# Kernel optimization log

Measured on AMD Instinct MI355X. Metric: run time of the kernel, lower is better.

## Reference

```python
import jax, jax.numpy as jnp
import numpy as np


def setup_inputs() -> dict:
    key = jax.random.key(0)
    k1, k2, k3, k4 = jax.random.split(key, 4)
    B, L, F, V = 512, 512, 64, 20000
    src_ids = jax.random.randint(k1, (B, L), 0, V, dtype=jnp.int32)
    dst_ids = jax.random.randint(k2, (B, L), 0, V, dtype=jnp.int32)
    # MLP params: Linear(1->F), ReLU, Linear(F->F)
    W1 = jax.random.normal(k3, (1, F), dtype=jnp.float32)  # fan_in = 1
    b1 = jnp.zeros((F,), dtype=jnp.float32)
    W2 = jax.random.normal(k4, (F, F), dtype=jnp.float32) * (1.0 / np.sqrt(F))
    b2 = jnp.zeros((F,), dtype=jnp.float32)
    return {"src_ids": src_ids, "dst_ids": dst_ids, "W1": W1, "b1": b1,
            "W2": W2, "b2": b2, "num_nodes": V}


def reference(src_ids, dst_ids, W1, b1, W2, b2, num_nodes):
    # Per-row histogram over node ids (vectorized replacement for
    # np.unique + dict gather in the torch code).
    row_hist = lambda r: jnp.bincount(r, length=num_nodes)
    hist_src = jax.vmap(row_hist)(src_ids)  # [B, V]
    hist_dst = jax.vmap(row_hist)(dst_ids)  # [B, V]

    gather = lambda h, ids: jnp.take_along_axis(h, ids, axis=1)  # [B, L]

    # appearances: [count in own seq, count in other seq], shape [B, L, 2]
    src_app = jnp.stack([gather(hist_src, src_ids), gather(hist_dst, src_ids)], axis=-1).astype(jnp.float32)
    dst_app = jnp.stack([gather(hist_src, dst_ids), gather(hist_dst, dst_ids)], axis=-1).astype(jnp.float32)
    # id 0 is padding -> zero both count channels
    src_app = jnp.where((src_ids == 0)[..., None], 0.0, src_app)
    dst_app = jnp.where((dst_ids == 0)[..., None], 0.0, dst_app)

    def encode(app):
        # app: [B, L, 2]; per-scalar MLP then sum over the 2 count channels
        h = jax.nn.relu(app[..., None] * W1[0] + b1)  # [B, L, 2, F]
        out = h @ W2 + b2                              # [B, L, 2, F]
        return out.sum(axis=2)                         # [B, L, F]

    return encode(src_app), encode(dst_app)
```

## Files before the change

kernel.cpp:

```cpp
#include <hip/hip_runtime.h>

constexpr int Bn = 512;
constexpr int Ln = 512;
constexpr int Fn = 64;
constexpr int Vn = 20000;
constexpr int HWORDS = (Vn + 2) / 3;

__global__ void build_table_kernel(const float* __restrict__ W1,
                                   const float* __restrict__ b1,
                                   const float* __restrict__ W2,
                                   const float* __restrict__ b2,
                                   float* __restrict__ table) {
    const int v = blockIdx.x;
    const int j = threadIdx.x;
    __shared__ float h[Fn];
    h[j] = fmaxf((float)v * W1[j] + b1[j], 0.0f);
    __syncthreads();
    float acc = b2[j];
#pragma unroll
    for (int i = 0; i < Fn; ++i)
        acc = fmaf(h[i], W2[i * Fn + j], acc);
    table[v * Fn + j] = acc;
}

__device__ __forceinline__ unsigned hist_get(const unsigned* __restrict__ h, int v) {
    const int w = v / 3;
    const int f = v - w * 3;
    return (h[w] >> (10 * f)) & 0x3FFu;
}

__global__ __launch_bounds__(256) void comco_kernel(
    const int* __restrict__ src_ids,
    const int* __restrict__ dst_ids,
    const float* __restrict__ table,
    float* __restrict__ out_src,
    float* __restrict__ out_dst) {
    __shared__ unsigned hs[HWORDS];
    __shared__ unsigned hd[HWORDS];

    const int b = blockIdx.x;
    const int tid = threadIdx.x;

    for (int i = tid; i < HWORDS; i += 256) { hs[i] = 0u; hd[i] = 0u; }
    __syncthreads();

    const int* __restrict__ srow = src_ids + b * Ln;
    const int* __restrict__ drow = dst_ids + b * Ln;

    for (int l = tid; l < Ln; l += 256) {
        const int s = srow[l];
        const int sw = s / 3;
        atomicAdd(&hs[sw], 1u << (10 * (s - sw * 3)));
        const int d = drow[l];
        const int dw = d / 3;
        atomicAdd(&hd[dw], 1u << (10 * (d - dw * 3)));
    }
    __syncthreads();

    const int g = tid >> 4;
    const int r = tid & 15;

    for (int l = g; l < Ln; l += 16) {
        const int sid = srow[l];
        const int did = drow[l];
        unsigned c_ss = 0, c_sd = 0, c_ds = 0, c_dd = 0;
        if (sid != 0) { c_ss = hist_get(hs, sid); c_sd = hist_get(hd, sid); }
        if (did != 0) { c_ds = hist_get(hs, did); c_dd = hist_get(hd, did); }

        const float4 t0 = *((const float4*)(table + c_ss * Fn) + r);
        const float4 t1 = *((const float4*)(table + c_sd * Fn) + r);
        const float4 u0 = *((const float4*)(table + c_ds * Fn) + r);
        const float4 u1 = *((const float4*)(table + c_dd * Fn) + r);

        float4 os, od;
        os.x = t0.x + t1.x; os.y = t0.y + t1.y; os.z = t0.z + t1.z; os.w = t0.w + t1.w;
        od.x = u0.x + u1.x; od.y = u0.y + u1.y; od.z = u0.z + u1.z; od.w = u0.w + u1.w;

        const size_t pos = (size_t)(b * Ln + l) * Fn;
        *((float4*)(out_src + pos) + r) = os;
        *((float4*)(out_dst + pos) + r) = od;
    }
}

extern "C" void kernel_launch(void* const* d_in, const int* in_sizes, int n_in,
                              void* d_out, int out_size, void* d_ws, size_t ws_size,
                              hipStream_t stream) {
    const int*   src_ids = (const int*)d_in[0];
    const int*   dst_ids = (const int*)d_in[1];
    const float* W1      = (const float*)d_in[2];
    const float* b1      = (const float*)d_in[3];
    const float* W2      = (const float*)d_in[4];
    const float* b2      = (const float*)d_in[5];

    float* table   = (float*)d_ws;
    float* out_src = (float*)d_out;
    float* out_dst = out_src + (size_t)Bn * Ln * Fn;

    build_table_kernel<<<Ln + 1, Fn, 0, stream>>>(W1, b1, W2, b2, table);
    comco_kernel<<<Bn, 256, 0, stream>>>(src_ids, dst_ids, table, out_src, out_dst);
}
```

Measured before the change: 150.1 us.

## Split histogram and output expansion into separate kernels via packed count buffer

The fused per-row kernel is split in two. A histogram kernel writes packed (own, other) counts per token to a workspace buffer, and a fully parallel expand kernel then gathers the two table rows and writes the output with one float4 per thread across the whole grid. This targets the low parallelism of the write phase, where 512 blocks each looped over 512 positions, and should let the large output store saturate bandwidth. The cost is an extra launch plus a small intermediate write and read of counts.

```diff
diff --git a/kernel.cpp b/kernel.cpp
--- a/kernel.cpp
+++ b/kernel.cpp
@@ -5,6 +5,7 @@
 constexpr int Fn = 64;
 constexpr int Vn = 20000;
 constexpr int HWORDS = (Vn + 2) / 3;
+constexpr int BL = Bn * Ln;
 
 __global__ void build_table_kernel(const float* __restrict__ W1,
                                    const float* __restrict__ b1,
@@ -29,12 +30,10 @@
     return (h[w] >> (10 * f)) & 0x3FFu;
 }
 
-__global__ __launch_bounds__(256) void comco_kernel(
+__global__ __launch_bounds__(256) void hist_kernel(
     const int* __restrict__ src_ids,
     const int* __restrict__ dst_ids,
-    const float* __restrict__ table,
-    float* __restrict__ out_src,
-    float* __restrict__ out_dst) {
+    unsigned* __restrict__ counts) {
     __shared__ unsigned hs[HWORDS];
     __shared__ unsigned hd[HWORDS];
 
@@ -47,39 +46,46 @@
     const int* __restrict__ srow = src_ids + b * Ln;
     const int* __restrict__ drow = dst_ids + b * Ln;
 
-    for (int l = tid; l < Ln; l += 256) {
-        const int s = srow[l];
-        const int sw = s / 3;
-        atomicAdd(&hs[sw], 1u << (10 * (s - sw * 3)));
-        const int d = drow[l];
-        const int dw = d / 3;
-        atomicAdd(&hd[dw], 1u << (10 * (d - dw * 3)));
+    const int s0 = srow[tid], s1 = srow[tid + 256];
+    const int d0 = drow[tid], d1 = drow[tid + 256];
+    {
+        int w;
+        w = s0 / 3; atomicAdd(&hs[w], 1u << (10 * (s0 - w * 3)));
+        w = s1 / 3; atomicAdd(&hs[w], 1u << (10 * (s1 - w * 3)));
+        w = d0 / 3; atomicAdd(&hd[w], 1u << (10 * (d0 - w * 3)));
+        w = d1 / 3; atomicAdd(&hd[w], 1u << (10 * (d1 - w * 3)));
     }
     __syncthreads();
 
-    const int g = tid >> 4;
-    const int r = tid & 15;
+    const size_t base = (size_t)b * Ln;
+#pragma unroll
+    for (int k = 0; k < 2; ++k) {
+        const int l = tid + k * 256;
+        const int s = (k == 0) ? s0 : s1;
+        const int d = (k == 0) ? d0 : d1;
+        unsigned ws = 0u, wd = 0u;
+        if (s != 0) ws = hist_get(hs, s) | (hist_get(hd, s) << 16);
+        if (d != 0) wd = hist_get(hs, d) | (hist_get(hd, d) << 16);
+        counts[base + l] = ws;
+        counts[BL + base + l] = wd;
+    }
+}
 
-    for (int l = g; l < Ln; l += 16) {
-        const int sid = srow[l];
-        const int did = drow[l];
-        unsigned c_ss = 0, c_sd = 0, c_ds = 0, c_dd = 0;
-        if (sid != 0) { c_ss = hist_get(hs, sid); c_sd = hist_get(hd, sid); }
-        if (did != 0) { c_ds = hist_get(hs, did); c_dd = hist_get(hd, did); }
-
-        const float4 t0 = *((const float4*)(table + c_ss * Fn) + r);
-        const float4 t1 = *((const float4*)(table + c_sd * Fn) + r);
-        const float4 u0 = *((const float4*)(table + c_ds * Fn) + r);
-        const float4 u1 = *((const float4*)(table + c_dd * Fn) + r);
-
-        float4 os, od;
-        os.x = t0.x + t1.x; os.y = t0.y + t1.y; os.z = t0.z + t1.z; os.w = t0.w + t1.w;
-        od.x = u0.x + u1.x; od.y = u0.y + u1.y; od.z = u0.z + u1.z; od.w = u0.w + u1.w;
-
-        const size_t pos = (size_t)(b * Ln + l) * Fn;
-        *((float4*)(out_src + pos) + r) = os;
-        *((float4*)(out_dst + pos) + r) = od;
-    }
+__global__ __launch_bounds__(256) void expand_kernel(
+    const unsigned* __restrict__ counts,
+    const float* __restrict__ table,
+    float* __restrict__ out) {
+    const unsigned g = blockIdx.x * 256u + threadIdx.x;
+    const unsigned r = g & 15u;
+    const unsigned idx = g >> 4;
+    const unsigned w = counts[idx];
+    const unsigned c0 = w & 0xFFFFu;
+    const unsigned c1 = w >> 16;
+    const float4 t0 = *((const float4*)(table + c0 * Fn) + r);
+    const float4 t1 = *((const float4*)(table + c1 * Fn) + r);
+    float4 o;
+    o.x = t0.x + t1.x; o.y = t0.y + t1.y; o.z = t0.z + t1.z; o.w = t0.w + t1.w;
+    *((float4*)(out + (size_t)idx * Fn) + r) = o;
 }
 
 extern "C" void kernel_launch(void* const* d_in, const int* in_sizes, int n_in,
@@ -92,10 +98,10 @@
     const float* W2      = (const float*)d_in[4];
     const float* b2      = (const float*)d_in[5];
 
-    float* table   = (float*)d_ws;
-    float* out_src = (float*)d_out;
-    float* out_dst = out_src + (size_t)Bn * Ln * Fn;
+    float*    table  = (float*)d_ws;
+    unsigned* counts = (unsigned*)(table + 513 * Fn);
 
     build_table_kernel<<<Ln + 1, Fn, 0, stream>>>(W1, b1, W2, b2, table);
-    comco_kernel<<<Bn, 256, 0, stream>>>(src_ids, dst_ids, table, out_src, out_dst);
+    hist_kernel<<<Bn, 256, 0, stream>>>(src_ids, dst_ids, counts);
+    expand_kernel<<<(2 * BL * 16) / 256, 256, 0, stream>>>(counts, table, (float*)d_out);
 }
```

After: 149.9 us. No clear change (-0.1%).
